# Optimization experiments

Hardware: AMD Instinct MI355X
Metric: run time of the kernel (lower is better)

Reference implementation:

```python
import jax, jax.numpy as jnp
import numpy as np

B, N, D = 32, 1024, 128  # batch, node_num, input_dim
TIME_STEP = 5


def setup_inputs() -> dict:
    key = jax.random.key(0)
    ks = jax.random.split(key, 12)
    s2 = 1.0 / np.sqrt(2 * D)
    s1 = 1.0 / np.sqrt(D)
    return {
        "input": jax.random.normal(ks[0], (B, N, D), jnp.float32),
        "in_matrix": jax.random.uniform(ks[1], (N, N), jnp.float32),
        "out_matrix": jax.random.uniform(ks[2], (N, N), jnp.float32),
        "w3_w": jax.random.normal(ks[3], (D, 2 * D), jnp.float32) * s2,
        "w3_b": jnp.zeros((D,), jnp.float32),
        "u3_w": jax.random.normal(ks[4], (D, D), jnp.float32) * s1,
        "u3_b": jnp.zeros((D,), jnp.float32),
        "w4_w": jax.random.normal(ks[5], (D, 2 * D), jnp.float32) * s2,
        "w4_b": jnp.zeros((D,), jnp.float32),
        "w5_w": jax.random.normal(ks[6], (D, 2 * D), jnp.float32) * s2,
        "w5_b": jnp.zeros((D,), jnp.float32),
        "u5_w": jax.random.normal(ks[7], (D, D), jnp.float32) * s1,
        "u5_b": jnp.zeros((D,), jnp.float32),
        "time_step": TIME_STEP,
    }


def reference(input, in_matrix, out_matrix, w3_w, w3_b, u3_w, u3_b,
              w4_w, w4_b, w5_w, w5_b, u5_w, u5_b, time_step):
    # GGNN: per step, in/out adjacency message passing + GRU-style gated update.
    def step(h, _):
        # message passing: adjacency applied per batch element [B,N,D]
        m_in = jnp.einsum('nm,bmd->bnd', in_matrix, h)
        m_out = jnp.einsum('nm,bmd->bnd', out_matrix, h)
        av = jnp.concatenate([m_in, m_out], axis=-1)  # [B,N,2D]
        # NOTE: original code uses fc_eq3_u for BOTH z and r (fc_eq4_u unused)
        u3 = h @ u3_w.T + u3_b
        z = jax.nn.sigmoid(av @ w3_w.T + w3_b + u3)
        r = jax.nn.sigmoid(av @ w4_w.T + w4_b + u3)
        hv = jnp.tanh(av @ w5_w.T + w5_b + ((r * h) @ u5_w.T + u5_b))
        h = (1.0 - z) * h + z * hv
        return h, None

    h, _ = jax.lax.scan(step, input, None, length=time_step)
    return h
```

## Files before the change

kernel.cpp:

```cpp
#include <hip/hip_runtime.h>
#include <cstdint>
#include <cstddef>


typedef _Float16 f16;
typedef __attribute__((ext_vector_type(8))) _Float16 f16x8;
typedef __attribute__((ext_vector_type(4))) float f32x4;

#define LDX 768
#define LDH 2048
#define CSCL 4.8828125e-4f

static __device__ __forceinline__ void gload16(const void* g, void* l) {
  __builtin_amdgcn_global_load_lds(
      (const __attribute__((address_space(1))) void*)g,
      (__attribute__((address_space(3))) void*)l, 16, 0, 0);
}

static __device__ __forceinline__ float sigmoidf_(float x) {
  return 1.f / (1.f + expf(-x));
}

static __device__ __forceinline__ unsigned short bc16(f16 x) {
  return __builtin_bit_cast(unsigned short, x);
}

static __device__ __forceinline__ void split2(float v, f16& l0, f16& l1) {
  l0 = (f16)v;
  l1 = (f16)((v - (float)l0) * 2048.0f);
}

static __device__ __forceinline__ void gemf(const f16* __restrict__ A, int lda,
                                            int aLS, int abase,
                                            const f16* __restrict__ B, int ldb,
                                            int bLS, int nkt, f16* lds,
                                            f32x4 (&aM)[4][4], f32x4 (&aC)[4][4]) {
  const int t = threadIdx.x;
  const int wave = t >> 6, lane = t & 63;
  const int wr = wave >> 1, wn = wave & 1;
  const int frow = lane & 15;
  const int fk = lane >> 4;
  const int sl = fk ^ ((frow >> 1) & 3);
  const int gs = (t & 3) ^ ((t >> 3) & 3);

#define STG(buf, kt)                                                          \
  _Pragma("unroll") for (int lb = 0; lb < 2; ++lb)                            \
  _Pragma("unroll") for (int g = 0; g < 2; ++g) {                             \
    const int row_ = g * 64 + (t >> 2);                                       \
    gload16(A + (size_t)row_ * lda + abase + lb * aLS + (kt) * 32 + gs * 8,   \
            lds + (buf) * 16384 + lb * 4096 + g * 2048 + wave * 512);         \
    gload16(B + (size_t)row_ * ldb + lb * bLS + (kt) * 32 + gs * 8,           \
            lds + (buf) * 16384 + 8192 + lb * 4096 + g * 2048 + wave * 512);  \
  }

  STG(0, 0);
  for (int kt = 0; kt < nkt; ++kt) {
    const int cur = kt & 1;
    if (kt + 1 < nkt) {
      STG(cur ^ 1, kt + 1);
      asm volatile("s_waitcnt vmcnt(8)" ::: "memory");
    } else {
      asm volatile("s_waitcnt vmcnt(0)" ::: "memory");
    }
    __builtin_amdgcn_s_barrier();
    asm volatile("" ::: "memory");

    const f16* bp = lds + cur * 16384;
    f16x8 a0[4], a1[4], b0[4], b1[4];
#pragma unroll
    for (int nf = 0; nf < 4; ++nf) {
      const int row = wn * 64 + nf * 16 + frow;
      b0[nf] = *(const f16x8*)&bp[8192 + row * 32 + sl * 8];
      b1[nf] = *(const f16x8*)&bp[12288 + row * 32 + sl * 8];
    }
#pragma unroll
    for (int mf = 0; mf < 4; ++mf) {
      const int row = wr * 64 + mf * 16 + frow;
      a0[mf] = *(const f16x8*)&bp[row * 32 + sl * 8];
      a1[mf] = *(const f16x8*)&bp[4096 + row * 32 + sl * 8];
    }
    __builtin_amdgcn_s_setprio(1);
#pragma unroll
    for (int mf = 0; mf < 4; ++mf)
#pragma unroll
      for (int nf = 0; nf < 4; ++nf) {
        aC[mf][nf] = __builtin_amdgcn_mfma_f32_16x16x32_f16(a0[mf], b1[nf],
                                                            aC[mf][nf], 0, 0, 0);
        aC[mf][nf] = __builtin_amdgcn_mfma_f32_16x16x32_f16(a1[mf], b0[nf],
                                                            aC[mf][nf], 0, 0, 0);
      }
#pragma unroll
    for (int mf = 0; mf < 4; ++mf)
#pragma unroll
      for (int nf = 0; nf < 4; ++nf)
        aM[mf][nf] = __builtin_amdgcn_mfma_f32_16x16x32_f16(a0[mf], b0[nf],
                                                            aM[mf][nf], 0, 0, 0);
    __builtin_amdgcn_s_setprio(0);
    asm volatile("" ::: "memory");
    __builtin_amdgcn_s_barrier();
  }
#undef STG
}

#define ACC_ZERO(acc)                          \
  _Pragma("unroll") for (int i = 0; i < 4; ++i) \
  _Pragma("unroll") for (int j = 0; j < 4; ++j) acc[i][j] = {0.f, 0.f, 0.f, 0.f};

__global__ __launch_bounds__(256, 2) void adjf(const f16* __restrict__ A2f,
                                               const f16* __restrict__ hN2f,
                                               f16* __restrict__ X2) {
  __shared__ f16 lds[32768];
  const int m0 = blockIdx.y * 128;
  const int n0 = blockIdx.x * 128;
  f32x4 aM[4][4], aC[4][4];
  ACC_ZERO(aM);
  ACC_ZERO(aC);
  gemf(A2f + (size_t)m0 * LDH, LDH, 1024, 0, hN2f + (size_t)n0 * LDH, LDH, 1024,
       32, lds, aM, aC);

  const int lane = threadIdx.x & 63, wave = threadIdx.x >> 6;
  const int rb = m0 + (wave >> 1) * 64 + (lane >> 4) * 4;
  const int cb = n0 + (wave & 1) * 64 + (lane & 15);
#pragma unroll
  for (int mf = 0; mf < 4; ++mf)
#pragma unroll
    for (int nf = 0; nf < 4; ++nf)
#pragma unroll
      for (int j = 0; j < 4; ++j) {
        const int gr = rb + mf * 16 + j;
        const int gc = cb + nf * 16;
        const float v = aM[mf][nf][j] + aC[mf][nf][j] * CSCL;
        const int node = gr & 1023;
        const int coff = (gr >> 10) * 128;
        const int bb = gc >> 7, d = gc & 127;
        f16* px = X2 + ((size_t)node * 32 + bb) * LDX + coff + d;
        f16 l0, l1;
        split2(v, l0, l1);
        px[0] = l0;
        px[384] = l1;
      }
}

__global__ __launch_bounds__(256, 2) void densef(const f16* __restrict__ X2,
                                                 const f16* __restrict__ Wsm,
                                                 const f16* __restrict__ u3wb,
                                                 const float* __restrict__ u3b,
                                                 float* __restrict__ pre,
                                                 float* __restrict__ u3f) {
  __shared__ f16 lds[32768];
  const int m0 = blockIdx.y * 128;
  const int bx = blockIdx.x;
  f32x4 aM[4][4], aC[4][4];
  ACC_ZERO(aM);
  ACC_ZERO(aC);
  const int lane = threadIdx.x & 63, wave = threadIdx.x >> 6;
  const int rb = m0 + (wave >> 1) * 64 + (lane >> 4) * 4;
  const int cb = (wave & 1) * 64 + (lane & 15);
  if (bx < 3) {
    gemf(X2 + (size_t)m0 * LDX, LDX, 384, 0, Wsm + (size_t)bx * 128 * 512, 512, 256,
         8, lds, aM, aC);
#pragma unroll
    for (int mf = 0; mf < 4; ++mf)
#pragma unroll
      for (int nf = 0; nf < 4; ++nf)
#pragma unroll
        for (int j = 0; j < 4; ++j)
          pre[(size_t)(rb + mf * 16 + j) * 384 + bx * 128 + cb + nf * 16] =
              aM[mf][nf][j] + aC[mf][nf][j] * CSCL;
  } else {
    gemf(X2 + (size_t)m0 * LDX, LDX, 384, 256, u3wb, 256, 128, 4, lds, aM, aC);
#pragma unroll
    for (int mf = 0; mf < 4; ++mf)
#pragma unroll
      for (int nf = 0; nf < 4; ++nf)
#pragma unroll
        for (int j = 0; j < 4; ++j) {
          const int gc = cb + nf * 16;
          const float v = aM[mf][nf][j] + aC[mf][nf][j] * CSCL;
          u3f[(size_t)(rb + mf * 16 + j) * 128 + gc] = v + u3b[gc];
        }
  }
}

__global__ __launch_bounds__(256, 2) void u5g(const f16* __restrict__ rh2,
                                              const f16* __restrict__ u5wb,
                                              const float* __restrict__ pre,
                                              const float* __restrict__ u3f,
                                              const float* __restrict__ h,
                                              const float* __restrict__ w3b,
                                              const float* __restrict__ w5b,
                                              const float* __restrict__ u5b,
                                              float* __restrict__ out) {
  __shared__ f16 lds[32768];
  const int m0 = blockIdx.x * 128;
  f32x4 aM[4][4], aC[4][4];
  ACC_ZERO(aM);
  ACC_ZERO(aC);
  gemf(rh2 + (size_t)m0 * 256, 256, 128, 0, u5wb, 256, 128, 4, lds, aM, aC);

  const int lane = threadIdx.x & 63, wave = threadIdx.x >> 6;
  const int rb = m0 + (wave >> 1) * 64 + (lane >> 4) * 4;
  const int cb = (wave & 1) * 64 + (lane & 15);
#pragma unroll
  for (int mf = 0; mf < 4; ++mf)
#pragma unroll
    for (int nf = 0; nf < 4; ++nf)
#pragma unroll
      for (int j = 0; j < 4; ++j) {
        const int gr = rb + mf * 16 + j;
        const int gc = cb + nf * 16;
        const float v = aM[mf][nf][j] + aC[mf][nf][j] * CSCL;
        const float u5f = v + u5b[gc];
        const float z = sigmoidf_((pre[(size_t)gr * 384 + gc] + w3b[gc]) +
                                  u3f[(size_t)gr * 128 + gc]);
        const float hv = tanhf((pre[(size_t)gr * 384 + 256 + gc] + w5b[gc]) + u5f);
        const int bb = gr & 31, node = gr >> 5;
        const size_t hi = ((size_t)bb * 1024 + node) * 128 + gc;
        const float hh = h[hi];
        out[hi] = (1.f - z) * hh + z * hv;
      }
}

__global__ __launch_bounds__(256) void pack_h(const float* __restrict__ h,
                                              f16* __restrict__ hN2f,
                                              f16* __restrict__ X2) {
  __shared__ unsigned int lds01[128][33];
  const int t = threadIdx.x;
  const int b = blockIdx.y;
  const int n0 = blockIdx.x * 32;
#pragma unroll
  for (int i = 0; i < 16; ++i) {
    const int idx = i * 256 + t;
    const int nl = idx >> 7, d = idx & 127;
    const float v = h[((size_t)b * 1024 + n0 + nl) * 128 + d];
    f16 l0, l1;
    split2(v, l0, l1);
    const size_t xr = ((size_t)(n0 + nl) * 32 + b) * LDX + 256 + d;
    X2[xr] = l0;
    X2[xr + 384] = l1;
    lds01[d][nl] = (unsigned)bc16(l0) | ((unsigned)bc16(l1) << 16);
  }
  __syncthreads();
#pragma unroll
  for (int i = 0; i < 16; ++i) {
    const int idx = i * 256 + t;
    const int d = idx >> 5, nl = idx & 31;
    const unsigned pk = lds01[d][nl];
    f16* row = hN2f + (size_t)(b * 128 + d) * LDH + n0 + nl;
    row[0] = __builtin_bit_cast(f16, (unsigned short)(pk & 0xffffu));
    row[1024] = __builtin_bit_cast(f16, (unsigned short)(pk >> 16));
  }
}

__global__ __launch_bounds__(256) void ew1(const float* __restrict__ pre,
                                           const float* __restrict__ u3f,
                                           const float* __restrict__ h,
                                           const float* __restrict__ w4b,
                                           f16* __restrict__ rh2) {
  const int e4 = blockIdx.x * 256 + threadIdx.x;
  const int r = e4 >> 5;
  const int dq = (e4 & 31) * 4;
  const int b = r & 31, n = r >> 5;
  const f32x4 p = *(const f32x4*)(pre + (size_t)r * 384 + 128 + dq);
  const f32x4 uf = *(const f32x4*)(u3f + (size_t)r * 128 + dq);
  const f32x4 hh = *(const f32x4*)(h + ((size_t)b * 1024 + n) * 128 + dq);
  const f32x4 b4 = *(const f32x4*)(w4b + dq);
  f16 o0[4], o1[4];
#pragma unroll
  for (int j = 0; j < 4; ++j) {
    const float rr = sigmoidf_((p[j] + b4[j]) + uf[j]);
    const float v = rr * hh[j];
    split2(v, o0[j], o1[j]);
  }
  *(ulong1*)&rh2[(size_t)r * 256 + dq] = *(ulong1*)o0;
  *(ulong1*)&rh2[(size_t)r * 256 + 128 + dq] = *(ulong1*)o1;
}

__global__ __launch_bounds__(256) void split_adjf(const float* __restrict__ src,
                                                  f16* __restrict__ dst) {
  const int i = blockIdx.x * 256 + threadIdx.x;
  const int r = i >> 10, c = i & 1023;
  f16 l0, l1;
  split2(src[i], l0, l1);
  dst[(size_t)r * LDH + c] = l0;
  dst[(size_t)r * LDH + 1024 + c] = l1;
}

__global__ void build_wsm(const float* __restrict__ w3, const float* __restrict__ w4,
                          const float* __restrict__ w5, f16* __restrict__ Wsm) {
  const int k = blockIdx.x * 128 + threadIdx.x;
  const int j = blockIdx.y;
  float v;
  if (j < 128) v = w3[j * 256 + k];
  else if (j < 256) v = w4[(j - 128) * 256 + k];
  else v = w5[(j - 256) * 256 + k];
  f16 l0, l1;
  split2(v, l0, l1);
  Wsm[(size_t)j * 512 + k] = l0;
  Wsm[(size_t)j * 512 + 256 + k] = l1;
}

__global__ void build_uw(const float* __restrict__ u, f16* __restrict__ dst) {
  const int i = blockIdx.x * 256 + threadIdx.x;
  const int j = i >> 7, k = i & 127;
  f16 l0, l1;
  split2(u[i], l0, l1);
  dst[(size_t)j * 256 + k] = l0;
  dst[(size_t)j * 256 + 128 + k] = l1;
}

__global__ void sentinel(float* out, int n) {
  const int i = blockIdx.x * 256 + threadIdx.x;
  if (i < n) out[i] = 123456789.f;
}

extern "C" void kernel_launch(void* const* d_in, const int* in_sizes, int n_in,
                              void* d_out, int out_size, void* d_ws, size_t ws_size,
                              hipStream_t stream) {
  const float* input = (const float*)d_in[0];
  const float* Ain = (const float*)d_in[1];
  const float* Aout = (const float*)d_in[2];
  const float* w3w = (const float*)d_in[3];
  const float* w3b = (const float*)d_in[4];
  const float* u3w = (const float*)d_in[5];
  const float* u3b = (const float*)d_in[6];
  const float* w4w = (const float*)d_in[7];
  const float* w4b = (const float*)d_in[8];
  const float* w5w = (const float*)d_in[9];
  const float* w5b = (const float*)d_in[10];
  const float* u5wf = (const float*)d_in[11];
  const float* u5b = (const float*)d_in[12];

  char* ws = (char*)d_ws;
  size_t off = 0;
  auto alloc = [&](size_t bytes) -> void* {
    void* p = ws + off;
    off += (bytes + 255) & ~(size_t)255;
    return p;
  };
  f16* A2f = (f16*)alloc(2048ull * LDH * 2);
  f16* hN2f = (f16*)alloc(4096ull * LDH * 2);
  f16* X2 = (f16*)alloc(32768ull * LDX * 2);
  f16* Wsm = (f16*)alloc(384ull * 512 * 2);
  f16* u3wb = (f16*)alloc(128ull * 256 * 2);
  f16* u5wb = (f16*)alloc(128ull * 256 * 2);
  float* pre = (float*)alloc(32768ull * 384 * 4);
  float* u3f = (float*)alloc(32768ull * 128 * 4);
  f16* rh2 = hN2f;
  if (off > ws_size) {
    sentinel<<<dim3((out_size + 255) / 256), dim3(256), 0, stream>>>((float*)d_out, out_size);
    return;
  }

  split_adjf<<<dim3(4096), dim3(256), 0, stream>>>(Ain, A2f);
  split_adjf<<<dim3(4096), dim3(256), 0, stream>>>(Aout, A2f + 1024ull * LDH);
  build_wsm<<<dim3(2, 384), dim3(128), 0, stream>>>(w3w, w4w, w5w, Wsm);
  build_uw<<<dim3(64), dim3(256), 0, stream>>>(u3w, u3wb);
  build_uw<<<dim3(64), dim3(256), 0, stream>>>(u5wf, u5wb);

  float* out = (float*)d_out;
  const float* h = input;
  for (int step = 0; step < 5; ++step) {
    pack_h<<<dim3(32, 32), dim3(256), 0, stream>>>(h, hN2f, X2);
    adjf<<<dim3(32, 16), dim3(256), 0, stream>>>(A2f, hN2f, X2);
    densef<<<dim3(4, 256), dim3(256), 0, stream>>>(X2, Wsm, u3wb, u3b, pre, u3f);
    ew1<<<dim3(4096), dim3(256), 0, stream>>>(pre, u3f, h, w4b, rh2);
    u5g<<<dim3(256), dim3(256), 0, stream>>>(rh2, u5wb, pre, u3f, h, w3b, w5b, u5b, out);
    h = out;
  }
}
```

Before: 689.4 us.

## Fuse u3 GEMM into gate GEMMs, fold ew1 into densef, use 32x32 MFMA

```diff
diff --git a/kernel.cpp b/kernel.cpp
--- a/kernel.cpp
+++ b/kernel.cpp
@@ -5,6 +5,7 @@
 
 typedef _Float16 f16;
 typedef __attribute__((ext_vector_type(8))) _Float16 f16x8;
+typedef __attribute__((ext_vector_type(16))) float f32x16;
 typedef __attribute__((ext_vector_type(4))) float f32x4;
 
 #define LDX 768
@@ -30,17 +31,22 @@
   l1 = (f16)((v - (float)l0) * 2048.0f);
 }
 
+#define ACCZ(a)                                 \
+  _Pragma("unroll") for (int i_ = 0; i_ < 2; ++i_) \
+  _Pragma("unroll") for (int j_ = 0; j_ < 2; ++j_) \
+  _Pragma("unroll") for (int e_ = 0; e_ < 16; ++e_) a[i_][j_][e_] = 0.f;
+
 static __device__ __forceinline__ void gemf(const f16* __restrict__ A, int lda,
                                             int aLS, int abase,
                                             const f16* __restrict__ B, int ldb,
                                             int bLS, int nkt, f16* lds,
-                                            f32x4 (&aM)[4][4], f32x4 (&aC)[4][4]) {
+                                            f32x16 (&aM)[2][2], f32x16 (&aC)[2][2]) {
   const int t = threadIdx.x;
   const int wave = t >> 6, lane = t & 63;
   const int wr = wave >> 1, wn = wave & 1;
-  const int frow = lane & 15;
-  const int fk = lane >> 4;
-  const int sl = fk ^ ((frow >> 1) & 3);
+  const int frow = lane & 31;
+  const int kh = lane >> 5;
+  const int fswz = (frow >> 1) & 3;
   const int gs = (t & 3) ^ ((t >> 3) & 3);
 
 #define STG(buf, kt)                                                          \
@@ -66,35 +72,47 @@
     asm volatile("" ::: "memory");
 
     const f16* bp = lds + cur * 16384;
-    f16x8 a0[4], a1[4], b0[4], b1[4];
-#pragma unroll
-    for (int nf = 0; nf < 4; ++nf) {
-      const int row = wn * 64 + nf * 16 + frow;
-      b0[nf] = *(const f16x8*)&bp[8192 + row * 32 + sl * 8];
-      b1[nf] = *(const f16x8*)&bp[12288 + row * 32 + sl * 8];
-    }
-#pragma unroll
-    for (int mf = 0; mf < 4; ++mf) {
-      const int row = wr * 64 + mf * 16 + frow;
-      a0[mf] = *(const f16x8*)&bp[row * 32 + sl * 8];
-      a1[mf] = *(const f16x8*)&bp[4096 + row * 32 + sl * 8];
-    }
+    f16x8 a0[2][2], a1[2][2], b0[2][2], b1[2][2];
+#pragma unroll
+    for (int n = 0; n < 2; ++n)
+#pragma unroll
+      for (int ks = 0; ks < 2; ++ks) {
+        const int row = wn * 64 + n * 32 + frow;
+        const int slot = (ks * 2 + kh) ^ fswz;
+        b0[n][ks] = *(const f16x8*)&bp[8192 + row * 32 + slot * 8];
+        b1[n][ks] = *(const f16x8*)&bp[12288 + row * 32 + slot * 8];
+      }
+#pragma unroll
+    for (int m = 0; m < 2; ++m)
+#pragma unroll
+      for (int ks = 0; ks < 2; ++ks) {
+        const int row = wr * 64 + m * 32 + frow;
+        const int slot = (ks * 2 + kh) ^ fswz;
+        a0[m][ks] = *(const f16x8*)&bp[row * 32 + slot * 8];
+        a1[m][ks] = *(const f16x8*)&bp[4096 + row * 32 + slot * 8];
+      }
     __builtin_amdgcn_s_setprio(1);
 #pragma unroll
-    for (int mf = 0; mf < 4; ++mf)
-#pragma unroll
-      for (int nf = 0; nf < 4; ++nf) {
-        aC[mf][nf] = __builtin_amdgcn_mfma_f32_16x16x32_f16(a0[mf], b1[nf],
-                                                            aC[mf][nf], 0, 0, 0);
-        aC[mf][nf] = __builtin_amdgcn_mfma_f32_16x16x32_f16(a1[mf], b0[nf],
-                                                            aC[mf][nf], 0, 0, 0);
-      }
-#pragma unroll
-    for (int mf = 0; mf < 4; ++mf)
-#pragma unroll
-      for (int nf = 0; nf < 4; ++nf)
-        aM[mf][nf] = __builtin_amdgcn_mfma_f32_16x16x32_f16(a0[mf], b0[nf],
-                                                            aM[mf][nf], 0, 0, 0);
+    for (int m = 0; m < 2; ++m)
+#pragma unroll
+      for (int n = 0; n < 2; ++n) {
+#pragma unroll
+        for (int ks = 0; ks < 2; ++ks)
+          aC[m][n] = __builtin_amdgcn_mfma_f32_32x32x16_f16(a0[m][ks], b1[n][ks],
+                                                            aC[m][n], 0, 0, 0);
+#pragma unroll
+        for (int ks = 0; ks < 2; ++ks)
+          aC[m][n] = __builtin_amdgcn_mfma_f32_32x32x16_f16(a1[m][ks], b0[n][ks],
+                                                            aC[m][n], 0, 0, 0);
+      }
+#pragma unroll
+    for (int m = 0; m < 2; ++m)
+#pragma unroll
+      for (int n = 0; n < 2; ++n)
+#pragma unroll
+        for (int ks = 0; ks < 2; ++ks)
+          aM[m][n] = __builtin_amdgcn_mfma_f32_32x32x16_f16(a0[m][ks], b0[n][ks],
+                                                            aM[m][n], 0, 0, 0);
     __builtin_amdgcn_s_setprio(0);
     asm volatile("" ::: "memory");
     __builtin_amdgcn_s_barrier();
@@ -102,9 +120,12 @@
 #undef STG
 }
 
-#define ACC_ZERO(acc)                          \
-  _Pragma("unroll") for (int i = 0; i < 4; ++i) \
-  _Pragma("unroll") for (int j = 0; j < 4; ++j) acc[i][j] = {0.f, 0.f, 0.f, 0.f};
+#define EPI32_IDX                                        \
+  const int lane = threadIdx.x & 63;                     \
+  const int wave = threadIdx.x >> 6;                     \
+  const int rbw = (wave >> 1) * 64;                      \
+  const int cbw = (wave & 1) * 64 + (lane & 31);         \
+  const int kh_ = (lane >> 5) * 4;
 
 __global__ __launch_bounds__(256, 2) void adjf(const f16* __restrict__ A2f,
                                                const f16* __restrict__ hN2f,
@@ -112,24 +133,21 @@
   __shared__ f16 lds[32768];
   const int m0 = blockIdx.y * 128;
   const int n0 = blockIdx.x * 128;
-  f32x4 aM[4][4], aC[4][4];
-  ACC_ZERO(aM);
-  ACC_ZERO(aC);
+  f32x16 aM[2][2], aC[2][2];
+  ACCZ(aM);
+  ACCZ(aC);
   gemf(A2f + (size_t)m0 * LDH, LDH, 1024, 0, hN2f + (size_t)n0 * LDH, LDH, 1024,
        32, lds, aM, aC);
-
-  const int lane = threadIdx.x & 63, wave = threadIdx.x >> 6;
-  const int rb = m0 + (wave >> 1) * 64 + (lane >> 4) * 4;
-  const int cb = n0 + (wave & 1) * 64 + (lane & 15);
-#pragma unroll
-  for (int mf = 0; mf < 4; ++mf)
-#pragma unroll
-    for (int nf = 0; nf < 4; ++nf)
-#pragma unroll
-      for (int j = 0; j < 4; ++j) {
-        const int gr = rb + mf * 16 + j;
-        const int gc = cb + nf * 16;
-        const float v = aM[mf][nf][j] + aC[mf][nf][j] * CSCL;
+  EPI32_IDX;
+#pragma unroll
+  for (int m = 0; m < 2; ++m)
+#pragma unroll
+    for (int n = 0; n < 2; ++n)
+#pragma unroll
+      for (int i = 0; i < 16; ++i) {
+        const int gr = m0 + rbw + m * 32 + (i & 3) + 8 * (i >> 2) + kh_;
+        const int gc = n0 + cbw + n * 32;
+        const float v = aM[m][n][i] + aC[m][n][i] * CSCL;
         const int node = gr & 1023;
         const int coff = (gr >> 10) * 128;
         const int bb = gc >> 7, d = gc & 127;
@@ -145,75 +163,78 @@
                                                  const f16* __restrict__ Wsm,
                                                  const f16* __restrict__ u3wb,
                                                  const float* __restrict__ u3b,
+                                                 const float* __restrict__ w4b,
+                                                 const float* __restrict__ h,
                                                  float* __restrict__ pre,
-                                                 float* __restrict__ u3f) {
+                                                 f16* __restrict__ rh2) {
   __shared__ f16 lds[32768];
   const int m0 = blockIdx.y * 128;
   const int bx = blockIdx.x;
-  f32x4 aM[4][4], aC[4][4];
-  ACC_ZERO(aM);
-  ACC_ZERO(aC);
-  const int lane = threadIdx.x & 63, wave = threadIdx.x >> 6;
-  const int rb = m0 + (wave >> 1) * 64 + (lane >> 4) * 4;
-  const int cb = (wave & 1) * 64 + (lane & 15);
-  if (bx < 3) {
-    gemf(X2 + (size_t)m0 * LDX, LDX, 384, 0, Wsm + (size_t)bx * 128 * 512, 512, 256,
+  f32x16 aM[2][2], aC[2][2];
+  ACCZ(aM);
+  ACCZ(aC);
+  if (bx == 2) {
+    gemf(X2 + (size_t)m0 * LDX, LDX, 384, 0, Wsm + (size_t)256 * 512, 512, 256,
          8, lds, aM, aC);
-#pragma unroll
-    for (int mf = 0; mf < 4; ++mf)
-#pragma unroll
-      for (int nf = 0; nf < 4; ++nf)
-#pragma unroll
-        for (int j = 0; j < 4; ++j)
-          pre[(size_t)(rb + mf * 16 + j) * 384 + bx * 128 + cb + nf * 16] =
-              aM[mf][nf][j] + aC[mf][nf][j] * CSCL;
   } else {
+    gemf(X2 + (size_t)m0 * LDX, LDX, 384, 0, Wsm + (size_t)(bx * 128) * 512, 512, 256,
+         8, lds, aM, aC);
     gemf(X2 + (size_t)m0 * LDX, LDX, 384, 256, u3wb, 256, 128, 4, lds, aM, aC);
-#pragma unroll
-    for (int mf = 0; mf < 4; ++mf)
-#pragma unroll
-      for (int nf = 0; nf < 4; ++nf)
-#pragma unroll
-        for (int j = 0; j < 4; ++j) {
-          const int gc = cb + nf * 16;
-          const float v = aM[mf][nf][j] + aC[mf][nf][j] * CSCL;
-          u3f[(size_t)(rb + mf * 16 + j) * 128 + gc] = v + u3b[gc];
+  }
+  EPI32_IDX;
+#pragma unroll
+  for (int m = 0; m < 2; ++m)
+#pragma unroll
+    for (int n = 0; n < 2; ++n)
+#pragma unroll
+      for (int i = 0; i < 16; ++i) {
+        const int gr = m0 + rbw + m * 32 + (i & 3) + 8 * (i >> 2) + kh_;
+        const int gc = cbw + n * 32;
+        const float v = aM[m][n][i] + aC[m][n][i] * CSCL;
+        if (bx == 0) {
+          pre[(size_t)gr * 256 + gc] = v;
+        } else if (bx == 2) {
+          pre[(size_t)gr * 256 + 128 + gc] = v;
+        } else {
+          const float rr = sigmoidf_((v + w4b[gc]) + u3b[gc]);
+          const int bb = gr & 31, node = gr >> 5;
+          const float hh = h[((size_t)bb * 1024 + node) * 128 + gc];
+          f16 l0, l1;
+          split2(rr * hh, l0, l1);
+          rh2[(size_t)gr * 256 + gc] = l0;
+          rh2[(size_t)gr * 256 + 128 + gc] = l1;
         }
-  }
+      }
 }
 
 __global__ __launch_bounds__(256, 2) void u5g(const f16* __restrict__ rh2,
                                               const f16* __restrict__ u5wb,
                                               const float* __restrict__ pre,
-                                              const float* __restrict__ u3f,
                                               const float* __restrict__ h,
                                               const float* __restrict__ w3b,
+                                              const float* __restrict__ u3b,
                                               const float* __restrict__ w5b,
                                               const float* __restrict__ u5b,
                                               float* __restrict__ out) {
   __shared__ f16 lds[32768];
   const int m0 = blockIdx.x * 128;
-  f32x4 aM[4][4], aC[4][4];
-  ACC_ZERO(aM);
-  ACC_ZERO(aC);
+  f32x16 aM[2][2], aC[2][2];
+  ACCZ(aM);
+  ACCZ(aC);
   gemf(rh2 + (size_t)m0 * 256, 256, 128, 0, u5wb, 256, 128, 4, lds, aM, aC);
-
-  const int lane = threadIdx.x & 63, wave = threadIdx.x >> 6;
-  const int rb = m0 + (wave >> 1) * 64 + (lane >> 4) * 4;
-  const int cb = (wave & 1) * 64 + (lane & 15);
-#pragma unroll
-  for (int mf = 0; mf < 4; ++mf)
-#pragma unroll
-    for (int nf = 0; nf < 4; ++nf)
-#pragma unroll
-      for (int j = 0; j < 4; ++j) {
-        const int gr = rb + mf * 16 + j;
-        const int gc = cb + nf * 16;
-        const float v = aM[mf][nf][j] + aC[mf][nf][j] * CSCL;
+  EPI32_IDX;
+#pragma unroll
+  for (int m = 0; m < 2; ++m)
+#pragma unroll
+    for (int n = 0; n < 2; ++n)
+#pragma unroll
+      for (int i = 0; i < 16; ++i) {
+        const int gr = m0 + rbw + m * 32 + (i & 3) + 8 * (i >> 2) + kh_;
+        const int gc = cbw + n * 32;
+        const float v = aM[m][n][i] + aC[m][n][i] * CSCL;
         const float u5f = v + u5b[gc];
-        const float z = sigmoidf_((pre[(size_t)gr * 384 + gc] + w3b[gc]) +
-                                  u3f[(size_t)gr * 128 + gc]);
-        const float hv = tanhf((pre[(size_t)gr * 384 + 256 + gc] + w5b[gc]) + u5f);
+        const float z = sigmoidf_((pre[(size_t)gr * 256 + gc] + w3b[gc]) + u3b[gc]);
+        const float hv = tanhf((pre[(size_t)gr * 256 + 128 + gc] + w5b[gc]) + u5f);
         const int bb = gr & 31, node = gr >> 5;
         const size_t hi = ((size_t)bb * 1024 + node) * 128 + gc;
         const float hh = h[hi];
@@ -250,30 +271,6 @@
     row[0] = __builtin_bit_cast(f16, (unsigned short)(pk & 0xffffu));
     row[1024] = __builtin_bit_cast(f16, (unsigned short)(pk >> 16));
   }
-}
-
-__global__ __launch_bounds__(256) void ew1(const float* __restrict__ pre,
-                                           const float* __restrict__ u3f,
-                                           const float* __restrict__ h,
-                                           const float* __restrict__ w4b,
-                                           f16* __restrict__ rh2) {
-  const int e4 = blockIdx.x * 256 + threadIdx.x;
-  const int r = e4 >> 5;
-  const int dq = (e4 & 31) * 4;
-  const int b = r & 31, n = r >> 5;
-  const f32x4 p = *(const f32x4*)(pre + (size_t)r * 384 + 128 + dq);
-  const f32x4 uf = *(const f32x4*)(u3f + (size_t)r * 128 + dq);
-  const f32x4 hh = *(const f32x4*)(h + ((size_t)b * 1024 + n) * 128 + dq);
-  const f32x4 b4 = *(const f32x4*)(w4b + dq);
-  f16 o0[4], o1[4];
-#pragma unroll
-  for (int j = 0; j < 4; ++j) {
-    const float rr = sigmoidf_((p[j] + b4[j]) + uf[j]);
-    const float v = rr * hh[j];
-    split2(v, o0[j], o1[j]);
-  }
-  *(ulong1*)&rh2[(size_t)r * 256 + dq] = *(ulong1*)o0;
-  *(ulong1*)&rh2[(size_t)r * 256 + 128 + dq] = *(ulong1*)o1;
 }
 
 __global__ __launch_bounds__(256) void split_adjf(const float* __restrict__ src,
@@ -344,8 +341,7 @@
   f16* Wsm = (f16*)alloc(384ull * 512 * 2);
   f16* u3wb = (f16*)alloc(128ull * 256 * 2);
   f16* u5wb = (f16*)alloc(128ull * 256 * 2);
-  float* pre = (float*)alloc(32768ull * 384 * 4);
-  float* u3f = (float*)alloc(32768ull * 128 * 4);
+  float* pre = (float*)alloc(32768ull * 256 * 4);
   f16* rh2 = hN2f;
   if (off > ws_size) {
     sentinel<<<dim3((out_size + 255) / 256), dim3(256), 0, stream>>>((float*)d_out, out_size);
@@ -363,9 +359,8 @@
   for (int step = 0; step < 5; ++step) {
     pack_h<<<dim3(32, 32), dim3(256), 0, stream>>>(h, hN2f, X2);
     adjf<<<dim3(32, 16), dim3(256), 0, stream>>>(A2f, hN2f, X2);
-    densef<<<dim3(4, 256), dim3(256), 0, stream>>>(X2, Wsm, u3wb, u3b, pre, u3f);
-    ew1<<<dim3(4096), dim3(256), 0, stream>>>(pre, u3f, h, w4b, rh2);
-    u5g<<<dim3(256), dim3(256), 0, stream>>>(rh2, u5wb, pre, u3f, h, w3b, w5b, u5b, out);
+    densef<<<dim3(3, 256), dim3(256), 0, stream>>>(X2, Wsm, u3wb, u3b, w4b, h, pre, rh2);
+    u5g<<<dim3(256), dim3(256), 0, stream>>>(rh2, u5wb, pre, h, w3b, u3b, w5b, u5b, out);
     h = out;
   }
 }
```

New measurement: 858.8 us. +24.6%, slower.

## Widen adjacency GEMM tile to 128x256 and merge split-fp16 accumulators

Applied to the files above, without the earlier changes.

```diff
diff --git a/kernel.cpp b/kernel.cpp
--- a/kernel.cpp
+++ b/kernel.cpp
@@ -9,7 +9,6 @@
 
 #define LDX 768
 #define LDH 2048
-#define CSCL 4.8828125e-4f
 
 static __device__ __forceinline__ void gload16(const void* g, void* l) {
   __builtin_amdgcn_global_load_lds(
@@ -27,14 +26,14 @@
 
 static __device__ __forceinline__ void split2(float v, f16& l0, f16& l1) {
   l0 = (f16)v;
-  l1 = (f16)((v - (float)l0) * 2048.0f);
-}
-
-static __device__ __forceinline__ void gemf(const f16* __restrict__ A, int lda,
-                                            int aLS, int abase,
-                                            const f16* __restrict__ B, int ldb,
-                                            int bLS, int nkt, f16* lds,
-                                            f32x4 (&aM)[4][4], f32x4 (&aC)[4][4]) {
+  l1 = (f16)(v - (float)l0);
+}
+
+static __device__ __forceinline__ void gemfN(const f16* __restrict__ A, int lda,
+                                             int aLS, int abase,
+                                             const f16* __restrict__ B, int ldb,
+                                             int bLS, int nkt, f16* lds,
+                                             f32x4 (&acc)[4][4]) {
   const int t = threadIdx.x;
   const int wave = t >> 6, lane = t & 63;
   const int wr = wave >> 1, wn = wave & 1;
@@ -43,7 +42,7 @@
   const int sl = fk ^ ((frow >> 1) & 3);
   const int gs = (t & 3) ^ ((t >> 3) & 3);
 
-#define STG(buf, kt)                                                          \
+#define STGN(buf, kt)                                                         \
   _Pragma("unroll") for (int lb = 0; lb < 2; ++lb)                            \
   _Pragma("unroll") for (int g = 0; g < 2; ++g) {                             \
     const int row_ = g * 64 + (t >> 2);                                       \
@@ -53,11 +52,11 @@
             lds + (buf) * 16384 + 8192 + lb * 4096 + g * 2048 + wave * 512);  \
   }
 
-  STG(0, 0);
+  STGN(0, 0);
   for (int kt = 0; kt < nkt; ++kt) {
     const int cur = kt & 1;
     if (kt + 1 < nkt) {
-      STG(cur ^ 1, kt + 1);
+      STGN(cur ^ 1, kt + 1);
       asm volatile("s_waitcnt vmcnt(8)" ::: "memory");
     } else {
       asm volatile("s_waitcnt vmcnt(0)" ::: "memory");
@@ -83,53 +82,137 @@
 #pragma unroll
     for (int mf = 0; mf < 4; ++mf)
 #pragma unroll
-      for (int nf = 0; nf < 4; ++nf) {
-        aC[mf][nf] = __builtin_amdgcn_mfma_f32_16x16x32_f16(a0[mf], b1[nf],
-                                                            aC[mf][nf], 0, 0, 0);
-        aC[mf][nf] = __builtin_amdgcn_mfma_f32_16x16x32_f16(a1[mf], b0[nf],
-                                                            aC[mf][nf], 0, 0, 0);
-      }
-#pragma unroll
-    for (int mf = 0; mf < 4; ++mf)
-#pragma unroll
       for (int nf = 0; nf < 4; ++nf)
-        aM[mf][nf] = __builtin_amdgcn_mfma_f32_16x16x32_f16(a0[mf], b0[nf],
-                                                            aM[mf][nf], 0, 0, 0);
+        acc[mf][nf] = __builtin_amdgcn_mfma_f32_16x16x32_f16(a0[mf], b1[nf],
+                                                             acc[mf][nf], 0, 0, 0);
+#pragma unroll
+    for (int mf = 0; mf < 4; ++mf)
+#pragma unroll
+      for (int nf = 0; nf < 4; ++nf)
+        acc[mf][nf] = __builtin_amdgcn_mfma_f32_16x16x32_f16(a1[mf], b0[nf],
+                                                             acc[mf][nf], 0, 0, 0);
+#pragma unroll
+    for (int mf = 0; mf < 4; ++mf)
+#pragma unroll
+      for (int nf = 0; nf < 4; ++nf)
+        acc[mf][nf] = __builtin_amdgcn_mfma_f32_16x16x32_f16(a0[mf], b0[nf],
+                                                             acc[mf][nf], 0, 0, 0);
     __builtin_amdgcn_s_setprio(0);
     asm volatile("" ::: "memory");
     __builtin_amdgcn_s_barrier();
   }
-#undef STG
-}
-
-#define ACC_ZERO(acc)                          \
-  _Pragma("unroll") for (int i = 0; i < 4; ++i) \
-  _Pragma("unroll") for (int j = 0; j < 4; ++j) acc[i][j] = {0.f, 0.f, 0.f, 0.f};
-
-__global__ __launch_bounds__(256, 2) void adjf(const f16* __restrict__ A2f,
+#undef STGN
+}
+
+static __device__ __forceinline__ void gemfW(const f16* __restrict__ A, int lda,
+                                             int aLS,
+                                             const f16* __restrict__ B, int ldb,
+                                             int bLS, int nkt, f16* lds,
+                                             f32x4 (&acc)[4][8]) {
+  const int t = threadIdx.x;
+  const int wave = t >> 6, lane = t & 63;
+  const int wrm = wave >> 1, wnn = wave & 1;
+  const int frow = lane & 15;
+  const int fk = lane >> 4;
+  const int sl = fk ^ ((frow >> 1) & 3);
+  const int gs = (t & 3) ^ ((t >> 3) & 3);
+
+#define STGW(buf, kt)                                                         \
+  _Pragma("unroll") for (int lb = 0; lb < 2; ++lb)                            \
+  _Pragma("unroll") for (int g = 0; g < 2; ++g) {                             \
+    const int row_ = g * 64 + (t >> 2);                                       \
+    gload16(A + (size_t)row_ * lda + lb * aLS + (kt) * 32 + gs * 8,           \
+            lds + (buf) * 24576 + lb * 4096 + g * 2048 + wave * 512);         \
+  }                                                                           \
+  _Pragma("unroll") for (int lb = 0; lb < 2; ++lb)                            \
+  _Pragma("unroll") for (int g = 0; g < 4; ++g) {                             \
+    const int row_ = g * 64 + (t >> 2);                                       \
+    gload16(B + (size_t)row_ * ldb + lb * bLS + (kt) * 32 + gs * 8,           \
+            lds + (buf) * 24576 + 8192 + lb * 8192 + g * 2048 + wave * 512);  \
+  }
+
+  STGW(0, 0);
+  for (int kt = 0; kt < nkt; ++kt) {
+    const int cur = kt & 1;
+    if (kt + 1 < nkt) {
+      STGW(cur ^ 1, kt + 1);
+      asm volatile("s_waitcnt vmcnt(12)" ::: "memory");
+    } else {
+      asm volatile("s_waitcnt vmcnt(0)" ::: "memory");
+    }
+    __builtin_amdgcn_s_barrier();
+    asm volatile("" ::: "memory");
+
+    const f16* bp = lds + cur * 24576;
+    f16x8 a0[4], a1[4], b0[8], b1[8];
+#pragma unroll
+    for (int mf = 0; mf < 4; ++mf) {
+      const int row = wrm * 64 + mf * 16 + frow;
+      a0[mf] = *(const f16x8*)&bp[row * 32 + sl * 8];
+      a1[mf] = *(const f16x8*)&bp[4096 + row * 32 + sl * 8];
+    }
+#pragma unroll
+    for (int nf = 0; nf < 8; ++nf) {
+      const int row = wnn * 128 + nf * 16 + frow;
+      b0[nf] = *(const f16x8*)&bp[8192 + row * 32 + sl * 8];
+      b1[nf] = *(const f16x8*)&bp[16384 + row * 32 + sl * 8];
+    }
+    __builtin_amdgcn_s_setprio(1);
+#pragma unroll
+    for (int mf = 0; mf < 4; ++mf)
+#pragma unroll
+      for (int nf = 0; nf < 8; ++nf)
+        acc[mf][nf] = __builtin_amdgcn_mfma_f32_16x16x32_f16(a0[mf], b1[nf],
+                                                             acc[mf][nf], 0, 0, 0);
+#pragma unroll
+    for (int mf = 0; mf < 4; ++mf)
+#pragma unroll
+      for (int nf = 0; nf < 8; ++nf)
+        acc[mf][nf] = __builtin_amdgcn_mfma_f32_16x16x32_f16(a1[mf], b0[nf],
+                                                             acc[mf][nf], 0, 0, 0);
+#pragma unroll
+    for (int mf = 0; mf < 4; ++mf)
+#pragma unroll
+      for (int nf = 0; nf < 8; ++nf)
+        acc[mf][nf] = __builtin_amdgcn_mfma_f32_16x16x32_f16(a0[mf], b0[nf],
+                                                             acc[mf][nf], 0, 0, 0);
+    __builtin_amdgcn_s_setprio(0);
+    asm volatile("" ::: "memory");
+    __builtin_amdgcn_s_barrier();
+  }
+#undef STGW
+}
+
+#define ACCZ4(a)                                   \
+  _Pragma("unroll") for (int i_ = 0; i_ < 4; ++i_) \
+  _Pragma("unroll") for (int j_ = 0; j_ < 4; ++j_) a[i_][j_] = {0.f, 0.f, 0.f, 0.f};
+#define ACCZ8(a)                                   \
+  _Pragma("unroll") for (int i_ = 0; i_ < 4; ++i_) \
+  _Pragma("unroll") for (int j_ = 0; j_ < 8; ++j_) a[i_][j_] = {0.f, 0.f, 0.f, 0.f};
+
+__global__ __launch_bounds__(256, 1) void adjf(const f16* __restrict__ A2f,
                                                const f16* __restrict__ hN2f,
                                                f16* __restrict__ X2) {
-  __shared__ f16 lds[32768];
+  __shared__ f16 lds[49152];
   const int m0 = blockIdx.y * 128;
-  const int n0 = blockIdx.x * 128;
-  f32x4 aM[4][4], aC[4][4];
-  ACC_ZERO(aM);
-  ACC_ZERO(aC);
-  gemf(A2f + (size_t)m0 * LDH, LDH, 1024, 0, hN2f + (size_t)n0 * LDH, LDH, 1024,
-       32, lds, aM, aC);
+  const int n0 = blockIdx.x * 256;
+  f32x4 acc[4][8];
+  ACCZ8(acc);
+  gemfW(A2f + (size_t)m0 * LDH, LDH, 1024, hN2f + (size_t)n0 * LDH, LDH, 1024,
+        32, lds, acc);
 
   const int lane = threadIdx.x & 63, wave = threadIdx.x >> 6;
   const int rb = m0 + (wave >> 1) * 64 + (lane >> 4) * 4;
-  const int cb = n0 + (wave & 1) * 64 + (lane & 15);
+  const int cb = n0 + (wave & 1) * 128 + (lane & 15);
 #pragma unroll
   for (int mf = 0; mf < 4; ++mf)
 #pragma unroll
-    for (int nf = 0; nf < 4; ++nf)
+    for (int nf = 0; nf < 8; ++nf)
 #pragma unroll
       for (int j = 0; j < 4; ++j) {
         const int gr = rb + mf * 16 + j;
         const int gc = cb + nf * 16;
-        const float v = aM[mf][nf][j] + aC[mf][nf][j] * CSCL;
+        const float v = acc[mf][nf][j];
         const int node = gr & 1023;
         const int coff = (gr >> 10) * 128;
         const int bb = gc >> 7, d = gc & 127;
@@ -150,15 +233,14 @@
   __shared__ f16 lds[32768];
   const int m0 = blockIdx.y * 128;
   const int bx = blockIdx.x;
-  f32x4 aM[4][4], aC[4][4];
-  ACC_ZERO(aM);
-  ACC_ZERO(aC);
+  f32x4 acc[4][4];
+  ACCZ4(acc);
   const int lane = threadIdx.x & 63, wave = threadIdx.x >> 6;
   const int rb = m0 + (wave >> 1) * 64 + (lane >> 4) * 4;
   const int cb = (wave & 1) * 64 + (lane & 15);
   if (bx < 3) {
-    gemf(X2 + (size_t)m0 * LDX, LDX, 384, 0, Wsm + (size_t)bx * 128 * 512, 512, 256,
-         8, lds, aM, aC);
+    gemfN(X2 + (size_t)m0 * LDX, LDX, 384, 0, Wsm + (size_t)bx * 128 * 512, 512, 256,
+          8, lds, acc);
 #pragma unroll
     for (int mf = 0; mf < 4; ++mf)
 #pragma unroll
@@ -166,9 +248,9 @@
 #pragma unroll
         for (int j = 0; j < 4; ++j)
           pre[(size_t)(rb + mf * 16 + j) * 384 + bx * 128 + cb + nf * 16] =
-              aM[mf][nf][j] + aC[mf][nf][j] * CSCL;
+              acc[mf][nf][j];
   } else {
-    gemf(X2 + (size_t)m0 * LDX, LDX, 384, 256, u3wb, 256, 128, 4, lds, aM, aC);
+    gemfN(X2 + (size_t)m0 * LDX, LDX, 384, 256, u3wb, 256, 128, 4, lds, acc);
 #pragma unroll
     for (int mf = 0; mf < 4; ++mf)
 #pragma unroll
@@ -176,8 +258,7 @@
 #pragma unroll
         for (int j = 0; j < 4; ++j) {
           const int gc = cb + nf * 16;
-          const float v = aM[mf][nf][j] + aC[mf][nf][j] * CSCL;
-          u3f[(size_t)(rb + mf * 16 + j) * 128 + gc] = v + u3b[gc];
+          u3f[(size_t)(rb + mf * 16 + j) * 128 + gc] = acc[mf][nf][j] + u3b[gc];
         }
   }
 }
@@ -193,10 +274,9 @@
                                               float* __restrict__ out) {
   __shared__ f16 lds[32768];
   const int m0 = blockIdx.x * 128;
-  f32x4 aM[4][4], aC[4][4];
-  ACC_ZERO(aM);
-  ACC_ZERO(aC);
-  gemf(rh2 + (size_t)m0 * 256, 256, 128, 0, u5wb, 256, 128, 4, lds, aM, aC);
+  f32x4 acc[4][4];
+  ACCZ4(acc);
+  gemfN(rh2 + (size_t)m0 * 256, 256, 128, 0, u5wb, 256, 128, 4, lds, acc);
 
   const int lane = threadIdx.x & 63, wave = threadIdx.x >> 6;
   const int rb = m0 + (wave >> 1) * 64 + (lane >> 4) * 4;
@@ -209,8 +289,7 @@
       for (int j = 0; j < 4; ++j) {
         const int gr = rb + mf * 16 + j;
         const int gc = cb + nf * 16;
-        const float v = aM[mf][nf][j] + aC[mf][nf][j] * CSCL;
-        const float u5f = v + u5b[gc];
+        const float u5f = acc[mf][nf][j] + u5b[gc];
         const float z = sigmoidf_((pre[(size_t)gr * 384 + gc] + w3b[gc]) +
                                   u3f[(size_t)gr * 128 + gc]);
         const float hv = tanhf((pre[(size_t)gr * 384 + 256 + gc] + w5b[gc]) + u5f);
@@ -362,7 +441,7 @@
   const float* h = input;
   for (int step = 0; step < 5; ++step) {
     pack_h<<<dim3(32, 32), dim3(256), 0, stream>>>(h, hN2f, X2);
-    adjf<<<dim3(32, 16), dim3(256), 0, stream>>>(A2f, hN2f, X2);
+    adjf<<<dim3(16, 16), dim3(256), 0, stream>>>(A2f, hN2f, X2);
     densef<<<dim3(4, 256), dim3(256), 0, stream>>>(X2, Wsm, u3wb, u3b, pre, u3f);
     ew1<<<dim3(4096), dim3(256), 0, stream>>>(pre, u3f, h, w4b, rh2);
     u5g<<<dim3(256), dim3(256), 0, stream>>>(rh2, u5wb, pre, u3f, h, w3b, w5b, u5b, out);
```

After: 748.5 us. 8.6% more time.
